# Kernel tuning notes

Hardware: AMD Instinct MI355X
Metric: run time of the kernel (lower is better)

Reference implementation:

```python
import jax, jax.numpy as jnp
import numpy as np

N = 100000       # nodes
E = 1600000      # edges (avg degree 16)
F_IN = 128       # feats_per_node
F1 = 128         # layer_1_feats
F2 = 128         # layer_2_feats


def setup_inputs() -> dict:
    key = jax.random.key(0)
    k1, k2, k3, k4, k5, k6 = jax.random.split(key, 6)
    node_feats = jax.random.normal(k1, (N, F_IN), dtype=jnp.float32)
    # COO representation of sparse normalized adjacency Ahat
    edge_rows = jax.random.randint(k2, (E,), 0, N)
    edge_cols = jax.random.randint(k3, (E,), 0, N)
    edge_vals = jax.random.uniform(k4, (E,), dtype=jnp.float32)
    # reset_param-style init: uniform in +-1/sqrt(fan_in)
    w0 = jax.random.uniform(k5, (F_IN, F1), dtype=jnp.float32,
                            minval=-1.0, maxval=1.0) / np.sqrt(F_IN)
    w1 = jax.random.uniform(k6, (F1, F2), dtype=jnp.float32,
                            minval=-1.0, maxval=1.0) / np.sqrt(F1)
    return {"node_feats": node_feats, "edge_vals": edge_vals,
            "w0": w0, "w1": w1,
            "edge_rows": edge_rows, "edge_cols": edge_cols}


def _spmm(edge_rows, edge_cols, edge_vals, x):
    # out[i] = sum_{(i,j) in edges} val_ij * x[j]   (Ahat @ x)
    msgs = edge_vals[:, None] * x[edge_cols]          # [E, F] gather
    return jax.ops.segment_sum(msgs, edge_rows, num_segments=N)


def reference(node_feats, edge_vals, w0, w1, edge_rows, edge_cols):
    # layer 0: relu(Ahat @ (X @ W0))
    h = jax.nn.relu(_spmm(edge_rows, edge_cols, edge_vals, node_feats @ w0))
    # layer 1: relu(Ahat @ (H @ W1))
    h = jax.nn.relu(_spmm(edge_rows, edge_cols, edge_vals, h @ w1))
    return h
```

## Files before the change

kernel.cpp:

```cpp
#include <hip/hip_runtime.h>

#define N_NODES 100000
#define N_EDGES 1600000
#define F 128
#define M_PAD 100032
#define GEMM_GRID 1563

#define BUCKET_BITS 9
#define BUCKET_SIZE 512
#define NBUCKETS 196
#define BCAP 9216
#define EPB_A 8192
#define ABLOCKS 196

#define AS1 __attribute__((address_space(1)))
#define AS3 __attribute__((address_space(3)))

typedef __attribute__((ext_vector_type(8))) short short8;
typedef __attribute__((ext_vector_type(4))) float f32x4;

__device__ __forceinline__ float bf_lo(unsigned int u) { return __uint_as_float(u << 16); }
__device__ __forceinline__ float bf_hi(unsigned int u) { return __uint_as_float(u & 0xffff0000u); }
__device__ __forceinline__ unsigned short f2bf(float f) {
    unsigned int u = __float_as_uint(f);
    u += 0x7fffu + ((u >> 16) & 1u);
    return (unsigned short)(u >> 16);
}
__device__ __forceinline__ void gload_lds16(const void* g, void* l) {
    __builtin_amdgcn_global_load_lds((const AS1 unsigned int*)g, (AS3 unsigned int*)l, 16, 0, 0);
}

__global__ __launch_bounds__(256) void prep_kernel(const float* __restrict__ W0,
                                                   const float* __restrict__ W1,
                                                   unsigned short* __restrict__ Wt0,
                                                   unsigned short* __restrict__ Wt1,
                                                   int* __restrict__ bucket_cursor) {
    int t = threadIdx.x;
    if (blockIdx.x == 2) {
        if (t < NBUCKETS) bucket_cursor[t] = 0;
        return;
    }
    const float* W = (blockIdx.x == 0) ? W0 : W1;
    unsigned short* Wt = (blockIdx.x == 0) ? Wt0 : Wt1;
    int c = t & 127;
    int o0 = (t >> 7) * 8;
    for (int o = o0; o < o0 + 8; ++o) {
        short8 v;
#pragma unroll
        for (int e = 0; e < 8; ++e) v[e] = (short)f2bf(W[(o * 8 + e) * 128 + c]);
        *(short8*)((char*)Wt + c * 256 + ((o * 16) ^ ((c & 7) << 4))) = v;
    }
}


__device__ __forceinline__ void binA_body(char* smem, int bid,
                                          const int* __restrict__ rows,
                                          const int* __restrict__ cols,
                                          const float* __restrict__ vals,
                                          int* __restrict__ bucket_cursor,
                                          uint2* __restrict__ stage) {
    int* hist = (int*)smem;
    int* base = hist + NBUCKETS;
    int tid = threadIdx.x;
    int start = bid * EPB_A;
    int cnt = min(EPB_A, N_EDGES - start);
    for (int i = tid; i < NBUCKETS; i += 256) hist[i] = 0;
    __syncthreads();
    for (int i = tid; i < cnt; i += 256) atomicAdd(&hist[rows[start + i] >> BUCKET_BITS], 1);
    __syncthreads();
    for (int i = tid; i < NBUCKETS; i += 256) {
        int h = hist[i];
        base[i] = h ? atomicAdd(&bucket_cursor[i], h) : 0;
        hist[i] = 0;
    }
    __syncthreads();
    for (int i = tid; i < cnt; i += 256) {
        int r = rows[start + i];
        int c = cols[start + i];
        unsigned vb = __float_as_uint(vals[start + i]);
        int b = r >> BUCKET_BITS;
        int p = b * BCAP + base[b] + atomicAdd(&hist[b], 1);
        stage[p] = make_uint2(((unsigned)(r & (BUCKET_SIZE - 1)) << 17) | (unsigned)c, vb);
    }
}

__device__ __forceinline__ void gemm0_body(char* smem, int bid,
                                           const float* __restrict__ X,
                                           const unsigned short* __restrict__ Wt0,
                                           unsigned short* __restrict__ T) {
    unsigned short* wlds = (unsigned short*)smem;
    unsigned short* alds = (unsigned short*)(smem + 32768);
    int tid = threadIdx.x;
    int w = tid >> 6, l = tid & 63;
    int q = l >> 4, c16 = l & 15;
    long r0 = (long)bid * 64;

#pragma unroll
    for (int i = 0; i < 8; ++i) {
        int row = w * 32 + i * 4 + q;
        gload_lds16((const char*)Wt0 + row * 256 + c16 * 16,
                    (char*)wlds + (w * 8192 + i * 1024));
    }
#pragma unroll
    for (int i = 0; i < 4; ++i) {
        int row = i * 16 + (tid >> 4);
        int oct = tid & 15;
        long rg = r0 + row;
        if (rg > N_NODES - 1) rg = N_NODES - 1;
        const float4* xp = (const float4*)(X + rg * 128 + oct * 8);
        float4 a = xp[0], bb = xp[1];
        short8 v;
        v[0] = (short)f2bf(a.x); v[1] = (short)f2bf(a.y);
        v[2] = (short)f2bf(a.z); v[3] = (short)f2bf(a.w);
        v[4] = (short)f2bf(bb.x); v[5] = (short)f2bf(bb.y);
        v[6] = (short)f2bf(bb.z); v[7] = (short)f2bf(bb.w);
        *(short8*)((char*)alds + row * 256 + ((oct * 16) ^ ((row & 7) << 4))) = v;
    }
    __syncthreads();

    f32x4 acc[8] = {};
    int nrow = w * 16 + c16;
    int nswz = (nrow & 7) << 4;
#pragma unroll
    for (int ks = 0; ks < 4; ++ks) {
        int kb = ks * 64 + q * 16;
        short8 bfrag = *(const short8*)((const char*)alds + nrow * 256 + (kb ^ nswz));
#pragma unroll
        for (int fb = 0; fb < 8; ++fb) {
            int frow = fb * 16 + c16;
            short8 afrag = *(const short8*)((const char*)wlds + frow * 256 +
                                            (kb ^ ((frow & 7) << 4)));
            acc[fb] = __builtin_amdgcn_mfma_f32_16x16x32_bf16(afrag, bfrag, acc[fb], 0, 0, 0);
        }
    }

    long node = r0 + w * 16 + c16;
#pragma unroll
    for (int fb = 0; fb < 8; ++fb) {
        uint2 o;
        o.x = (unsigned)f2bf(acc[fb][0]) | ((unsigned)f2bf(acc[fb][1]) << 16);
        o.y = (unsigned)f2bf(acc[fb][2]) | ((unsigned)f2bf(acc[fb][3]) << 16);
        *(uint2*)((char*)T + node * 256 + fb * 32 + q * 8) = o;
    }
}

__global__ __launch_bounds__(256) void k1_kernel(const float* __restrict__ X,
                                                 const unsigned short* __restrict__ Wt0,
                                                 unsigned short* __restrict__ T,
                                                 const int* __restrict__ rows,
                                                 const int* __restrict__ cols,
                                                 const float* __restrict__ vals,
                                                 int* __restrict__ bucket_cursor,
                                                 uint2* __restrict__ stage) {
    __shared__ char smem[49152];
    if (blockIdx.x < ABLOCKS) {
        binA_body(smem, blockIdx.x, rows, cols, vals, bucket_cursor, stage);
    } else {
        gemm0_body(smem, blockIdx.x - ABLOCKS, X, Wt0, T);
    }
}

__global__ __launch_bounds__(256) void mfma_gemm_kernel(const unsigned short* __restrict__ Av,
                                                        const unsigned short* __restrict__ Wt,
                                                        unsigned short* __restrict__ T) {
    __shared__ alignas(16) unsigned short wlds[128 * 128];
    __shared__ alignas(16) unsigned short alds[64 * 128];
    int tid = threadIdx.x;
    int w = tid >> 6, l = tid & 63;
    int q = l >> 4, c16 = l & 15;
    long r0 = (long)blockIdx.x * 64;

#pragma unroll
    for (int i = 0; i < 8; ++i) {
        int row = w * 32 + i * 4 + q;
        gload_lds16((const char*)Wt + row * 256 + c16 * 16,
                    (char*)wlds + (w * 8192 + i * 1024));
    }
#pragma unroll
    for (int i = 0; i < 4; ++i) {
        int row = w * 16 + i * 4 + q;
        gload_lds16((const char*)Av + (r0 + row) * 256 + c16 * 16,
                    (char*)alds + (w * 4096 + i * 1024));
    }
    __syncthreads();

    f32x4 acc[8] = {};
    int nrow = w * 16 + c16;
    int nswz = (nrow & 7) << 4;
#pragma unroll
    for (int ks = 0; ks < 4; ++ks) {
        int kb = ks * 64 + q * 16;
        short8 bfrag = *(const short8*)((const char*)alds + nrow * 256 + (kb ^ nswz));
#pragma unroll
        for (int fb = 0; fb < 8; ++fb) {
            int frow = fb * 16 + c16;
            short8 afrag = *(const short8*)((const char*)wlds + frow * 256 +
                                            (kb ^ ((frow & 7) << 4)));
            acc[fb] = __builtin_amdgcn_mfma_f32_16x16x32_bf16(afrag, bfrag, acc[fb], 0, 0, 0);
        }
    }

    long node = r0 + w * 16 + c16;
#pragma unroll
    for (int fb = 0; fb < 8; ++fb) {
        uint2 o;
        o.x = (unsigned)f2bf(acc[fb][0]) | ((unsigned)f2bf(acc[fb][1]) << 16);
        o.y = (unsigned)f2bf(acc[fb][2]) | ((unsigned)f2bf(acc[fb][3]) << 16);
        *(uint2*)((char*)T + node * 256 + fb * 32 + q * 8) = o;
    }
}

__global__ __launch_bounds__(1024) void binB_kernel(const uint2* __restrict__ stage,
                                                    const int* __restrict__ bucket_cursor,
                                                    uint2* __restrict__ csr,
                                                    uint2* __restrict__ rowseg) {
    __shared__ int hist[BUCKET_SIZE];
    __shared__ int scanv[BUCKET_SIZE];
    __shared__ int cur[BUCKET_SIZE];
    __shared__ int wsum[8], woff[8];
    int b = blockIdx.x;
    int t = threadIdx.x;
    int s0 = b * BCAP;
    int cnt = bucket_cursor[b];
    if (t < BUCKET_SIZE) hist[t] = 0;
    __syncthreads();
    for (int i = t; i < cnt; i += 1024) atomicAdd(&hist[stage[s0 + i].x >> 17], 1);
    __syncthreads();
    int wid = t >> 6, ln = t & 63;
    if (wid < 8) {
        int v = hist[wid * 64 + ln];
#pragma unroll
        for (int d = 1; d < 64; d <<= 1) {
            int u = __shfl_up(v, d);
            if (ln >= d) v += u;
        }
        if (ln == 63) wsum[wid] = v;
        scanv[wid * 64 + ln] = v;
    }
    __syncthreads();
    if (t == 0) {
        int run = 0;
#pragma unroll
        for (int i = 0; i < 8; ++i) { woff[i] = run; run += wsum[i]; }
    }
    __syncthreads();
    if (t < BUCKET_SIZE) {
        int incl = scanv[t] + woff[t >> 6];
        int st = s0 + incl - hist[t];
        cur[t] = st;
        int row = (b << BUCKET_BITS) + t;
        if (row < N_NODES) rowseg[row] = make_uint2((unsigned)st, (unsigned)(st + hist[t]));
    }
    __syncthreads();
    for (int i = t; i < cnt; i += 1024) {
        uint2 e = stage[s0 + i];
        int p = atomicAdd(&cur[e.x >> 17], 1);
        csr[p] = make_uint2(e.x & 0x1FFFFu, e.y);
    }
}

template <bool OUT_BF16>
__global__ __launch_bounds__(256) void spmm_relu_kernel(const uint2* __restrict__ rowseg,
                                                        const uint2* __restrict__ csr,
                                                        const uint2* __restrict__ T2,
                                                        void* __restrict__ outv) {
    int wave = threadIdx.x >> 6;
    int lane = threadIdx.x & 63;
    int half = lane >> 5;
    int fl = lane & 31;
    int row = blockIdx.x * 8 + wave * 2 + half;
    uint2 se = rowseg[row];
    int s = (int)se.x, e = (int)se.y;
    float a0 = 0.f, a1 = 0.f, a2 = 0.f, a3 = 0.f;
    for (int base = s; base < e; base += 32) {
        int cnt = min(32, e - base);
        uint2 ed = csr[base + fl];
        int col_l = (fl < cnt) ? (int)ed.x : 0;
        float val_l = (fl < cnt) ? __uint_as_float(ed.y) : 0.f;
        int rounds = (cnt + 3) >> 2;
        for (int r = 0; r < rounds; ++r) {
            int j = r * 4;
            int cc[4]; float vv[4]; uint2 xx[4];
#pragma unroll
            for (int i = 0; i < 4; ++i) {
                cc[i] = __shfl(col_l, j + i, 32);
                vv[i] = __shfl(val_l, j + i, 32);
            }
#pragma unroll
            for (int i = 0; i < 4; ++i) xx[i] = T2[cc[i] * 32 + fl];
#pragma unroll
            for (int i = 0; i < 4; ++i) {
                a0 = fmaf(vv[i], bf_lo(xx[i].x), a0);
                a1 = fmaf(vv[i], bf_hi(xx[i].x), a1);
                a2 = fmaf(vv[i], bf_lo(xx[i].y), a2);
                a3 = fmaf(vv[i], bf_hi(xx[i].y), a3);
            }
        }
    }
    a0 = fmaxf(a0, 0.f); a1 = fmaxf(a1, 0.f);
    a2 = fmaxf(a2, 0.f); a3 = fmaxf(a3, 0.f);
    if constexpr (OUT_BF16) {
        uint2 o;
        o.x = (unsigned)f2bf(a0) | ((unsigned)f2bf(a1) << 16);
        o.y = (unsigned)f2bf(a2) | ((unsigned)f2bf(a3) << 16);
        *(uint2*)((char*)outv + (size_t)row * 256 + ((fl * 8) ^ ((row & 7) << 4))) = o;
    } else {
        *(float4*)((float*)outv + (size_t)row * 128 + fl * 4) =
            make_float4(a0, a1, a2, a3);
    }
}

extern "C" void kernel_launch(void* const* d_in, const int* in_sizes, int n_in,
                              void* d_out, int out_size, void* d_ws, size_t ws_size,
                              hipStream_t stream) {
    const float* X     = (const float*)d_in[0];
    const float* evals = (const float*)d_in[1];
    const float* W0    = (const float*)d_in[2];
    const float* W1    = (const float*)d_in[3];
    const int* erows   = (const int*)d_in[4];
    const int* ecols   = (const int*)d_in[5];
    float* out = (float*)d_out;

    char* ws = (char*)d_ws;
    size_t off = 0;
    auto carve = [&](size_t bytes) {
        char* p = ws + off;
        off += (bytes + 255) & ~(size_t)255;
        return p;
    };
    unsigned short* T   = (unsigned short*)carve((size_t)M_PAD * F * 2);
    unsigned short* H   = (unsigned short*)carve((size_t)M_PAD * F * 2);
    unsigned short* Wt0 = (unsigned short*)carve(128 * 128 * 2);
    unsigned short* Wt1 = (unsigned short*)carve(128 * 128 * 2);
    uint2* stage        = (uint2*)carve((size_t)NBUCKETS * BCAP * 8);
    uint2* csr          = (uint2*)carve(((size_t)NBUCKETS * BCAP + 64) * 8);
    uint2* rowseg       = (uint2*)carve((size_t)N_NODES * 8);
    int* bucket_cursor  = (int*)carve((size_t)NBUCKETS * 4);
    (void)ws_size; (void)in_sizes; (void)n_in; (void)out_size;

    prep_kernel<<<3, 256, 0, stream>>>(W0, W1, Wt0, Wt1, bucket_cursor);

    k1_kernel<<<ABLOCKS + GEMM_GRID, 256, 0, stream>>>(X, Wt0, T, erows, ecols, evals,
                                                       bucket_cursor, stage);

    binB_kernel<<<NBUCKETS, 1024, 0, stream>>>(stage, bucket_cursor, csr, rowseg);

    spmm_relu_kernel<true><<<N_NODES / 8, 256, 0, stream>>>(rowseg, csr,
                                                            (const uint2*)T, H);

    mfma_gemm_kernel<<<GEMM_GRID, 256, 0, stream>>>(H, Wt1, T);

    spmm_relu_kernel<false><<<N_NODES / 8, 256, 0, stream>>>(rowseg, csr,
                                                             (const uint2*)T, out);
}
```

Measured before the change: 184.1 us.

## Fuse weight prep and CSR bucketing into one kernel with flag gates

Result: slower. 418.2 us (+127.1%).

```diff
diff --git a/kernel.cpp b/kernel.cpp
--- a/kernel.cpp
+++ b/kernel.cpp
@@ -13,6 +13,11 @@
 #define EPB_A 8192
 #define ABLOCKS 196
 
+#define K1_PREP 2
+#define K1_BINA (K1_PREP + ABLOCKS)
+#define K1_GEMM (K1_BINA + GEMM_GRID)
+#define K1_GRID (K1_GEMM + NBUCKETS)
+
 #define AS1 __attribute__((address_space(1)))
 #define AS3 __attribute__((address_space(3)))
 
@@ -30,18 +35,25 @@
     __builtin_amdgcn_global_load_lds((const AS1 unsigned int*)g, (AS3 unsigned int*)l, 16, 0, 0);
 }
 
-__global__ __launch_bounds__(256) void prep_kernel(const float* __restrict__ W0,
-                                                   const float* __restrict__ W1,
-                                                   unsigned short* __restrict__ Wt0,
-                                                   unsigned short* __restrict__ Wt1,
-                                                   int* __restrict__ bucket_cursor) {
+__device__ __forceinline__ void gate_wait(int* p, int v) {
+    if (threadIdx.x == 0) {
+        while (__hip_atomic_load(p, __ATOMIC_ACQUIRE, __HIP_MEMORY_SCOPE_AGENT) < v) {}
+        __threadfence();
+    }
+    __syncthreads();
+}
+__device__ __forceinline__ void gate_signal(int* p) {
+    __syncthreads();
+    if (threadIdx.x == 0) {
+        __threadfence();
+        __hip_atomic_fetch_add(p, 1, __ATOMIC_RELEASE, __HIP_MEMORY_SCOPE_AGENT);
+    }
+}
+
+
+__device__ __forceinline__ void prepW_body(int which, const float* __restrict__ W,
+                                           unsigned short* __restrict__ Wt) {
     int t = threadIdx.x;
-    if (blockIdx.x == 2) {
-        if (t < NBUCKETS) bucket_cursor[t] = 0;
-        return;
-    }
-    const float* W = (blockIdx.x == 0) ? W0 : W1;
-    unsigned short* Wt = (blockIdx.x == 0) ? Wt0 : Wt1;
     int c = t & 127;
     int o0 = (t >> 7) * 8;
     for (int o = o0; o < o0 + 8; ++o) {
@@ -51,7 +63,6 @@
         *(short8*)((char*)Wt + c * 256 + ((o * 16) ^ ((c & 7) << 4))) = v;
     }
 }
-
 
 __device__ __forceinline__ void binA_body(char* smem, int bid,
                                           const int* __restrict__ rows,
@@ -144,19 +155,86 @@
     }
 }
 
+__device__ __forceinline__ void binB_body(char* smem, int b,
+                                          const uint2* __restrict__ stage,
+                                          const int* __restrict__ bucket_cursor,
+                                          uint2* __restrict__ csr,
+                                          uint2* __restrict__ rowseg) {
+    int* hist = (int*)smem;
+    int* cur = hist + 512;
+    int* wsum = cur + 512;
+    int* woff = wsum + 4;
+    int t = threadIdx.x;
+    int s0 = b * BCAP;
+    int cnt = bucket_cursor[b];
+    hist[t] = 0; hist[t + 256] = 0;
+    __syncthreads();
+    for (int i = t; i < cnt; i += 256) atomicAdd(&hist[stage[s0 + i].x >> 17], 1);
+    __syncthreads();
+    int h0 = hist[2 * t], h1 = hist[2 * t + 1];
+    int psum = h0 + h1;
+    int ln = t & 63, wv = t >> 6;
+    int v = psum;
+#pragma unroll
+    for (int d = 1; d < 64; d <<= 1) {
+        int u = __shfl_up(v, d);
+        if (ln >= d) v += u;
+    }
+    if (ln == 63) wsum[wv] = v;
+    __syncthreads();
+    if (t == 0) {
+        int run = 0;
+#pragma unroll
+        for (int i = 0; i < 4; ++i) { woff[i] = run; run += wsum[i]; }
+    }
+    __syncthreads();
+    int excl = v + woff[wv] - psum;
+    int st0 = s0 + excl, st1 = st0 + h0;
+    cur[2 * t] = st0;
+    cur[2 * t + 1] = st1;
+    int row = (b << BUCKET_BITS) + 2 * t;
+    if (row < N_NODES) rowseg[row] = make_uint2((unsigned)st0, (unsigned)(st0 + h0));
+    if (row + 1 < N_NODES) rowseg[row + 1] = make_uint2((unsigned)st1, (unsigned)(st1 + h1));
+    __syncthreads();
+    for (int i = t; i < cnt; i += 256) {
+        uint2 e = stage[s0 + i];
+        int p = atomicAdd(&cur[e.x >> 17], 1);
+        csr[p] = make_uint2(e.x & 0x1FFFFu, e.y);
+    }
+}
+
 __global__ __launch_bounds__(256) void k1_kernel(const float* __restrict__ X,
-                                                 const unsigned short* __restrict__ Wt0,
+                                                 const float* __restrict__ W0,
+                                                 const float* __restrict__ W1,
+                                                 unsigned short* __restrict__ Wt0,
+                                                 unsigned short* __restrict__ Wt1,
                                                  unsigned short* __restrict__ T,
                                                  const int* __restrict__ rows,
                                                  const int* __restrict__ cols,
                                                  const float* __restrict__ vals,
                                                  int* __restrict__ bucket_cursor,
-                                                 uint2* __restrict__ stage) {
+                                                 uint2* __restrict__ stage,
+                                                 uint2* __restrict__ csr,
+                                                 uint2* __restrict__ rowseg,
+                                                 int* __restrict__ flags) {
     __shared__ char smem[49152];
-    if (blockIdx.x < ABLOCKS) {
-        binA_body(smem, blockIdx.x, rows, cols, vals, bucket_cursor, stage);
+    int bx = blockIdx.x;
+    if (bx < K1_PREP) {
+        if (bx == 0) {
+            prepW_body(0, W0, Wt0);
+            gate_signal(&flags[0]);
+        } else {
+            prepW_body(1, W1, Wt1);
+        }
+    } else if (bx < K1_BINA) {
+        binA_body(smem, bx - K1_PREP, rows, cols, vals, bucket_cursor, stage);
+        gate_signal(&flags[1]);
+    } else if (bx < K1_GEMM) {
+        gate_wait(&flags[0], 1);
+        gemm0_body(smem, bx - K1_BINA, X, Wt0, T);
     } else {
-        gemm0_body(smem, blockIdx.x - ABLOCKS, X, Wt0, T);
+        gate_wait(&flags[1], ABLOCKS);
+        binB_body(smem, bx - K1_GEMM, stage, bucket_cursor, csr, rowseg);
     }
 }
 
@@ -210,81 +288,48 @@
     }
 }
 
-__global__ __launch_bounds__(1024) void binB_kernel(const uint2* __restrict__ stage,
-                                                    const int* __restrict__ bucket_cursor,
-                                                    uint2* __restrict__ csr,
-                                                    uint2* __restrict__ rowseg) {
-    __shared__ int hist[BUCKET_SIZE];
-    __shared__ int scanv[BUCKET_SIZE];
-    __shared__ int cur[BUCKET_SIZE];
-    __shared__ int wsum[8], woff[8];
-    int b = blockIdx.x;
-    int t = threadIdx.x;
-    int s0 = b * BCAP;
-    int cnt = bucket_cursor[b];
-    if (t < BUCKET_SIZE) hist[t] = 0;
-    __syncthreads();
-    for (int i = t; i < cnt; i += 1024) atomicAdd(&hist[stage[s0 + i].x >> 17], 1);
-    __syncthreads();
-    int wid = t >> 6, ln = t & 63;
-    if (wid < 8) {
-        int v = hist[wid * 64 + ln];
-#pragma unroll
-        for (int d = 1; d < 64; d <<= 1) {
-            int u = __shfl_up(v, d);
-            if (ln >= d) v += u;
-        }
-        if (ln == 63) wsum[wid] = v;
-        scanv[wid * 64 + ln] = v;
-    }
-    __syncthreads();
-    if (t == 0) {
-        int run = 0;
-#pragma unroll
-        for (int i = 0; i < 8; ++i) { woff[i] = run; run += wsum[i]; }
-    }
-    __syncthreads();
-    if (t < BUCKET_SIZE) {
-        int incl = scanv[t] + woff[t >> 6];
-        int st = s0 + incl - hist[t];
-        cur[t] = st;
-        int row = (b << BUCKET_BITS) + t;
-        if (row < N_NODES) rowseg[row] = make_uint2((unsigned)st, (unsigned)(st + hist[t]));
-    }
-    __syncthreads();
-    for (int i = t; i < cnt; i += 1024) {
-        uint2 e = stage[s0 + i];
-        int p = atomicAdd(&cur[e.x >> 17], 1);
-        csr[p] = make_uint2(e.x & 0x1FFFFu, e.y);
-    }
-}
-
-template <bool OUT_BF16>
-__global__ __launch_bounds__(256) void spmm_relu_kernel(const uint2* __restrict__ rowseg,
-                                                        const uint2* __restrict__ csr,
-                                                        const uint2* __restrict__ T2,
-                                                        void* __restrict__ outv) {
-    int wave = threadIdx.x >> 6;
-    int lane = threadIdx.x & 63;
-    int half = lane >> 5;
-    int fl = lane & 31;
-    int row = blockIdx.x * 8 + wave * 2 + half;
-    uint2 se = rowseg[row];
+
+__device__ __forceinline__ void spmm_row(const uint2* __restrict__ csr,
+                                         const uint2* __restrict__ T2,
+                                         uint2 se, uint2 ed, int fl,
+                                         float& a0, float& a1, float& a2, float& a3) {
     int s = (int)se.x, e = (int)se.y;
-    float a0 = 0.f, a1 = 0.f, a2 = 0.f, a3 = 0.f;
-    for (int base = s; base < e; base += 32) {
-        int cnt = min(32, e - base);
-        uint2 ed = csr[base + fl];
-        int col_l = (fl < cnt) ? (int)ed.x : 0;
-        float val_l = (fl < cnt) ? __uint_as_float(ed.y) : 0.f;
-        int rounds = (cnt + 3) >> 2;
-        for (int r = 0; r < rounds; ++r) {
+    int cnt = min(32, e - s);
+    int col_l = (fl < cnt) ? (int)ed.x : 0;
+    float val_l = (fl < cnt) ? __uint_as_float(ed.y) : 0.f;
+    a0 = a1 = a2 = a3 = 0.f;
+    int rounds = (cnt + 3) >> 2;
+    for (int r = 0; r < rounds; ++r) {
+        int j = r * 4;
+        int cc[4]; float vv[4]; uint2 xx[4];
+#pragma unroll
+        for (int i = 0; i < 4; ++i) {
+            cc[i] = __shfl(col_l, j + i, 32);
+            vv[i] = __shfl(val_l, j + i, 32);
+        }
+#pragma unroll
+        for (int i = 0; i < 4; ++i) xx[i] = T2[cc[i] * 32 + fl];
+#pragma unroll
+        for (int i = 0; i < 4; ++i) {
+            a0 = fmaf(vv[i], bf_lo(xx[i].x), a0);
+            a1 = fmaf(vv[i], bf_hi(xx[i].x), a1);
+            a2 = fmaf(vv[i], bf_lo(xx[i].y), a2);
+            a3 = fmaf(vv[i], bf_hi(xx[i].y), a3);
+        }
+    }
+    for (int base = s + 32; base < e; base += 32) {
+        int c2 = min(32, e - base);
+        uint2 ed2 = csr[base + fl];
+        int col2 = (fl < c2) ? (int)ed2.x : 0;
+        float val2 = (fl < c2) ? __uint_as_float(ed2.y) : 0.f;
+        int r2 = (c2 + 3) >> 2;
+        for (int r = 0; r < r2; ++r) {
             int j = r * 4;
             int cc[4]; float vv[4]; uint2 xx[4];
 #pragma unroll
             for (int i = 0; i < 4; ++i) {
-                cc[i] = __shfl(col_l, j + i, 32);
-                vv[i] = __shfl(val_l, j + i, 32);
+                cc[i] = __shfl(col2, j + i, 32);
+                vv[i] = __shfl(val2, j + i, 32);
             }
 #pragma unroll
             for (int i = 0; i < 4; ++i) xx[i] = T2[cc[i] * 32 + fl];
@@ -297,6 +342,11 @@
             }
         }
     }
+}
+
+template <bool OUT_BF16>
+__device__ __forceinline__ void store_row(void* outv, int row, int fl,
+                                          float a0, float a1, float a2, float a3) {
     a0 = fmaxf(a0, 0.f); a1 = fmaxf(a1, 0.f);
     a2 = fmaxf(a2, 0.f); a3 = fmaxf(a3, 0.f);
     if constexpr (OUT_BF16) {
@@ -305,9 +355,35 @@
         o.y = (unsigned)f2bf(a2) | ((unsigned)f2bf(a3) << 16);
         *(uint2*)((char*)outv + (size_t)row * 256 + ((fl * 8) ^ ((row & 7) << 4))) = o;
     } else {
-        *(float4*)((float*)outv + (size_t)row * 128 + fl * 4) =
-            make_float4(a0, a1, a2, a3);
-    }
+        *(float4*)((float*)outv + (size_t)row * 128 + fl * 4) = make_float4(a0, a1, a2, a3);
+    }
+}
+
+template <bool OUT_BF16>
+__global__ __launch_bounds__(256) void spmm_relu_kernel(const uint2* __restrict__ rowseg,
+                                                        const uint2* __restrict__ csr,
+                                                        const uint2* __restrict__ T2,
+                                                        void* __restrict__ outv) {
+    int hw = threadIdx.x >> 5;
+    int fl = threadIdx.x & 31;
+    int r0 = (blockIdx.x * 8 + hw) * 4;
+    uint2 se0 = rowseg[r0 + 0];
+    uint2 se1 = rowseg[r0 + 1];
+    uint2 se2 = rowseg[r0 + 2];
+    uint2 se3 = rowseg[r0 + 3];
+    uint2 ed0 = csr[(int)se0.x + fl];
+    uint2 ed1 = csr[(int)se1.x + fl];
+    uint2 ed2 = csr[(int)se2.x + fl];
+    uint2 ed3 = csr[(int)se3.x + fl];
+    float a0, a1, a2, a3;
+    spmm_row(csr, T2, se0, ed0, fl, a0, a1, a2, a3);
+    store_row<OUT_BF16>(outv, r0 + 0, fl, a0, a1, a2, a3);
+    spmm_row(csr, T2, se1, ed1, fl, a0, a1, a2, a3);
+    store_row<OUT_BF16>(outv, r0 + 1, fl, a0, a1, a2, a3);
+    spmm_row(csr, T2, se2, ed2, fl, a0, a1, a2, a3);
+    store_row<OUT_BF16>(outv, r0 + 2, fl, a0, a1, a2, a3);
+    spmm_row(csr, T2, se3, ed3, fl, a0, a1, a2, a3);
+    store_row<OUT_BF16>(outv, r0 + 3, fl, a0, a1, a2, a3);
 }
 
 extern "C" void kernel_launch(void* const* d_in, const int* in_sizes, int n_in,
@@ -335,21 +411,22 @@
     uint2* stage        = (uint2*)carve((size_t)NBUCKETS * BCAP * 8);
     uint2* csr          = (uint2*)carve(((size_t)NBUCKETS * BCAP + 64) * 8);
     uint2* rowseg       = (uint2*)carve((size_t)N_NODES * 8);
-    int* bucket_cursor  = (int*)carve((size_t)NBUCKETS * 4);
+    int* ctrl           = (int*)carve((size_t)(NBUCKETS + 8) * 4);
     (void)ws_size; (void)in_sizes; (void)n_in; (void)out_size;
 
-    prep_kernel<<<3, 256, 0, stream>>>(W0, W1, Wt0, Wt1, bucket_cursor);
-
-    k1_kernel<<<ABLOCKS + GEMM_GRID, 256, 0, stream>>>(X, Wt0, T, erows, ecols, evals,
-                                                       bucket_cursor, stage);
-
-    binB_kernel<<<NBUCKETS, 1024, 0, stream>>>(stage, bucket_cursor, csr, rowseg);
-
-    spmm_relu_kernel<true><<<N_NODES / 8, 256, 0, stream>>>(rowseg, csr,
-                                                            (const uint2*)T, H);
+    int* bucket_cursor = ctrl;
+    int* flags = ctrl + NBUCKETS;
+
+    hipMemsetAsync(ctrl, 0, (size_t)(NBUCKETS + 8) * 4, stream);
+
+    k1_kernel<<<K1_GRID, 256, 0, stream>>>(X, W0, W1, Wt0, Wt1, T, erows, ecols, evals,
+                                           bucket_cursor, stage, csr, rowseg, flags);
+
+    spmm_relu_kernel<true><<<N_NODES / 32, 256, 0, stream>>>(rowseg, csr,
+                                                             (const uint2*)T, H);
 
     mfma_gemm_kernel<<<GEMM_GRID, 256, 0, stream>>>(H, Wt1, T);
 
-    spmm_relu_kernel<false><<<N_NODES / 8, 256, 0, stream>>>(rowseg, csr,
-                                                             (const uint2*)T, out);
-}
+    spmm_relu_kernel<false><<<N_NODES / 32, 256, 0, stream>>>(rowseg, csr,
+                                                              (const uint2*)T, out);
+}
```
